# Kernel tuning notes

Measured on AMD Instinct MI355X. Metric: run time of the kernel, lower is better.

## Reference

```python
import jax, jax.numpy as jnp
import numpy as np

EPS = 1e-5

def _ln(x, g, b):
    mu = jnp.mean(x, -1, keepdims=True)
    var = jnp.mean((x - mu) ** 2, -1, keepdims=True)
    return (x - mu) / jnp.sqrt(var + EPS) * g + b

def _edge_scores(x, lat, mask, sn_g, sn_b, tn_g, tn_b, su_w, su_b, tp_w, tp_b, m1_w, m1_b, m2_w, m2_b):
    # x: [B,S,D], lat: [B,K,D] -> edges [B,S,K]
    s = _ln(x, sn_g, sn_b) @ su_w + su_b      # [B,S,E]
    t = _ln(lat, tn_g, tn_b) @ tp_w + tp_b    # [B,K,E]
    B, S, E = s.shape
    K = t.shape[1]
    s4 = jnp.broadcast_to(s[:, :, None, :], (B, S, K, E))
    t4 = jnp.broadcast_to(t[:, None, :, :], (B, S, K, E))
    pair = jnp.concatenate([s4, t4, s4 * t4], axis=-1)  # [B,S,K,3E]
    h = jax.nn.gelu(pair @ m1_w + m1_b, approximate=False)
    e = (h @ m2_w + m2_b)[..., 0]             # [B,S,K]
    e = e / (1.0 + jnp.abs(e))                # softsign
    return e * mask[:, :, None]

def setup_inputs() -> dict:
    key = jax.random.key(0)
    B, St, Si, K, D, E = 2, 2048, 1024, 64, 768, 256
    ks = iter(jax.random.split(key, 64))
    d = {}
    d['text_values'] = jax.random.normal(next(ks), (B, St, D), jnp.float32)
    d['image_values'] = jax.random.normal(next(ks), (B, Si, D), jnp.float32)
    d['latent_state_init'] = jax.random.normal(next(ks), (B, K, D), jnp.float32)
    d['latent_value_init'] = jax.random.normal(next(ks), (B, K, D), jnp.float32)
    d['text_mask'] = jnp.ones((B, St), jnp.float32)
    d['image_mask'] = jnp.ones((B, Si), jnp.float32)
    def scorer(prefix):
        d[prefix + 'sn_g'] = jnp.ones((D,), jnp.float32)
        d[prefix + 'sn_b'] = jnp.zeros((D,), jnp.float32)
        d[prefix + 'tn_g'] = jnp.ones((D,), jnp.float32)
        d[prefix + 'tn_b'] = jnp.zeros((D,), jnp.float32)
        d[prefix + 'su_w'] = jax.random.normal(next(ks), (D, E), jnp.float32) * 0.02
        d[prefix + 'su_b'] = jnp.zeros((E,), jnp.float32)
        d[prefix + 'tp_w'] = jax.random.normal(next(ks), (D, E), jnp.float32) * 0.02
        d[prefix + 'tp_b'] = jnp.zeros((E,), jnp.float32)
        d[prefix + 'm1_w'] = jax.random.normal(next(ks), (3 * E, E), jnp.float32) * 0.02
        d[prefix + 'm1_b'] = jnp.zeros((E,), jnp.float32)
        d[prefix + 'm2_w'] = jax.random.normal(next(ks), (E, 1), jnp.float32) * 0.02
        d[prefix + 'm2_b'] = jnp.zeros((1,), jnp.float32)
    scorer('t_')
    scorer('i_')
    for p in ['tsn', 'isn', 'stn', 'vn']:
        d[p + '_g'] = jnp.ones((D,), jnp.float32)
        d[p + '_b'] = jnp.zeros((D,), jnp.float32)
    d['tsp_w'] = jax.random.normal(next(ks), (D, D), jnp.float32) * 0.02
    d['tsp_b'] = jnp.zeros((D,), jnp.float32)
    d['isp_w'] = jax.random.normal(next(ks), (D, D), jnp.float32) * 0.02
    d['isp_b'] = jnp.zeros((D,), jnp.float32)
    return d

def reference(text_values, image_values, latent_state_init, latent_value_init, text_mask, image_mask,
              t_sn_g, t_sn_b, t_tn_g, t_tn_b, t_su_w, t_su_b, t_tp_w, t_tp_b, t_m1_w, t_m1_b, t_m2_w, t_m2_b,
              i_sn_g, i_sn_b, i_tn_g, i_tn_b, i_su_w, i_su_b, i_tp_w, i_tp_b, i_m1_w, i_m1_b, i_m2_w, i_m2_b,
              tsn_g, tsn_b, isn_g, isn_b, stn_g, stn_b, vn_g, vn_b, tsp_w, tsp_b, isp_w, isp_b):
    t2l = _edge_scores(text_values, latent_value_init, text_mask,
                       t_sn_g, t_sn_b, t_tn_g, t_tn_b, t_su_w, t_su_b, t_tp_w, t_tp_b, t_m1_w, t_m1_b, t_m2_w, t_m2_b)
    i2l = _edge_scores(image_values, latent_value_init, image_mask,
                       i_sn_g, i_sn_b, i_tn_g, i_tn_b, i_su_w, i_su_b, i_tp_w, i_tp_b, i_m1_w, i_m1_b, i_m2_w, i_m2_b)
    tsf = _ln(text_values, tsn_g, tsn_b) @ tsp_w + tsp_b    # [B,St,D]
    isf = _ln(image_values, isn_g, isn_b) @ isp_w + isp_b   # [B,Si,D]
    state_raw = jnp.einsum('bsk,bsd->bkd', t2l, tsf) + jnp.einsum('bsk,bsd->bkd', i2l, isf)
    value_raw = jnp.einsum('bsk,bsd->bkd', t2l, text_values) + jnp.einsum('bsk,bsd->bkd', i2l, image_values)
    latent_state = _ln(state_raw + latent_state_init, stn_g, stn_b)
    latent_value = _ln(value_raw + latent_value_init, vn_g, vn_b)
    return latent_state, latent_value, t2l, i2l
```

## Files before the change

### kernel.cpp

```cpp
#include <hip/hip_runtime.h>
#include <math.h>

#define EPS_LN 1e-5f

#define B_  2
#define ST_ 2048
#define SI_ 1024
#define K_  64
#define D_  768
#define E_  256

typedef __bf16 bf16x8 __attribute__((ext_vector_type(8)));
typedef float  f32x4  __attribute__((ext_vector_type(4)));
typedef unsigned short ushort_t;

__device__ inline ushort_t f2bf(float x) {
    unsigned int u = __float_as_uint(x);
    unsigned int r = (u + 0x7FFFu + ((u >> 16) & 1u)) >> 16;
    return (ushort_t)r;
}

__device__ inline float gelu_fast(float z) {
    float a = fabsf(z);
    float t = __expf(a * -1.702f);
    float r = __builtin_amdgcn_rcpf(1.0f + t);
    float th = fmaf(t * r, -2.0f, 1.0f);
    return fmaf(0.5f * a, th, 0.5f * z);
}

__device__ void sgemm_acc_body(char* smem, int tid,
    const float* A, const float* Bm, const float* rowScale,
    const float* muA, const float* sdA, int so,
    float acc[4][4], int bx, int by, int k0beg, int k0end, int Kd, int N)
{
    float (*As)[65] = (float(*)[65])smem;
    float (*Bs)[64] = (float(*)[64])(smem + 16 * 65 * 4);
    int tx = tid & 15, ty = tid >> 4;
    int row0 = by * 64;
    int col0 = bx * 64;
    for (int k0 = k0beg; k0 < k0end; k0 += 16) {
        {
            int e = tid * 4;
            int r = e >> 4, kk = e & 15;
            float4 av = *(const float4*)(A + (size_t)(row0 + r) * Kd + k0 + kk);
            if (muA) {
                float m = muA[so + row0 + r], sd = sdA[so + row0 + r];
                av.x = (av.x - m) * sd; av.y = (av.y - m) * sd;
                av.z = (av.z - m) * sd; av.w = (av.w - m) * sd;
            }
            As[kk + 0][r] = av.x; As[kk + 1][r] = av.y; As[kk + 2][r] = av.z; As[kk + 3][r] = av.w;
        }
        {
            int e = tid * 4;
            int kk = e >> 6, c = e & 63;
            float4 bv = *(const float4*)(Bm + (size_t)(k0 + kk) * N + col0 + c);
            if (rowScale) {
                float sc = rowScale[k0 + kk];
                bv.x *= sc; bv.y *= sc; bv.z *= sc; bv.w *= sc;
            }
            *(float4*)&Bs[kk][c] = bv;
        }
        __syncthreads();
        #pragma unroll
        for (int kk = 0; kk < 16; ++kk) {
            float a[4], b[4];
            #pragma unroll
            for (int i = 0; i < 4; ++i) a[i] = As[kk][ty + 16 * i];
            #pragma unroll
            for (int j = 0; j < 4; ++j) b[j] = Bs[kk][tx + 16 * j];
            #pragma unroll
            for (int i = 0; i < 4; ++i)
                #pragma unroll
                for (int j = 0; j < 4; ++j)
                    acc[i][j] += a[i] * b[j];
        }
        __syncthreads();
    }
}

__global__ __launch_bounds__(256) void prelude_kernel(
    const float* __restrict__ xt, const float* __restrict__ xi,
    const float* __restrict__ lat,
    float* __restrict__ mu, float* __restrict__ rstd,
    const float* b0, const float* W0, const float* w0, float* f0,
    const float* b1, const float* W1, const float* w1, float* f1,
    const float* b2, const float* W2, const float* w2, float* f2,
    const float* b3, const float* W3, const float* w3, float* f3,
    const float* b4, const float* W4, const float* w4, float* f4,
    const float* b5, const float* W5, const float* w5, float* f5,
    const float* __restrict__ Wsu_t, const float* __restrict__ g_t, ushort_t* __restrict__ WF_t,
    const float* __restrict__ Wsu_i, const float* __restrict__ g_i, ushort_t* __restrict__ WF_i,
    const float* __restrict__ t_tp_w, const float* __restrict__ t_tn_g,
    const float* __restrict__ b_tp_t, float* __restrict__ t_t,
    const float* __restrict__ i_tp_w, const float* __restrict__ i_tn_g,
    const float* __restrict__ b_tp_i, float* __restrict__ t_i,
    float* __restrict__ rs_t, float* __restrict__ rs_i)
{
    extern __shared__ __align__(16) char smem[];
    int bid = blockIdx.x;
    int tid = threadIdx.x;
    if (bid < 16) {
        int bx = bid & 3, by = (bid >> 2) & 1, cfg = bid >> 3;
        float* smu = (float*)(smem + 8256);
        float* srs = smu + 64;
        int row0 = by * 64;
        {
            int r = tid >> 2, part = tid & 3;
            const float* xr = lat + (size_t)(row0 + r) * D_ + part * 192;
            float s = 0.f, q = 0.f;
            for (int i = 0; i < 192; i += 4) {
                float4 v = *(const float4*)(xr + i);
                s += v.x + v.y + v.z + v.w;
                q += v.x * v.x + v.y * v.y + v.z * v.z + v.w * v.w;
            }
            s += __shfl_xor(s, 1, 64); q += __shfl_xor(q, 1, 64);
            s += __shfl_xor(s, 2, 64); q += __shfl_xor(q, 2, 64);
            if (part == 0) {
                float m = s / (float)D_;
                smu[r] = m;
                srs[r] = rsqrtf(q / (float)D_ - m * m + EPS_LN);
            }
        }
        __syncthreads();
        float acc[4][4] = {};
        sgemm_acc_body(smem, tid, lat, cfg ? i_tp_w : t_tp_w, cfg ? i_tn_g : t_tn_g,
                       smu, srs, -row0, acc, bx, by, 0, D_, D_, E_);
        const float* bias = cfg ? b_tp_i : b_tp_t;
        float* C = cfg ? t_i : t_t;
        int tx = tid & 15, ty = tid >> 4;
        #pragma unroll
        for (int i = 0; i < 4; ++i) {
            int r = row0 + ty + 16 * i;
            #pragma unroll
            for (int j = 0; j < 4; ++j) {
                int c = bx * 64 + tx + 16 * j;
                C[(size_t)r * E_ + c] = acc[i][j] + bias[c];
            }
        }
        return;
    }
    if (bid < 56) {
        int f = bid - 16;
        int cfg, ebx;
        if (f < 16) { cfg = f >> 2; ebx = f & 3; }
        else { f -= 16; cfg = 4 + f / 12; ebx = f % 12; }
        const float* blns[6] = {b0, b1, b2, b3, b4, b5};
        const float* Ws[6]   = {W0, W1, W2, W3, W4, W5};
        const float* wbs[6]  = {w0, w1, w2, w3, w4, w5};
        float* bfs[6]        = {f0, f1, f2, f3, f4, f5};
        int E = (cfg >= 4) ? 768 : 256;
        const float* bln = blns[cfg];
        const float* W = Ws[cfg];
        float (*red)[64] = (float(*)[64])smem;
        int c = tid & 63, part = tid >> 6;
        int e = ebx * 64 + c;
        float s = 0.f;
        for (int d = part * 192; d < part * 192 + 192; ++d)
            s += bln[d] * W[(size_t)d * E + e];
        red[part][c] = s; __syncthreads();
        if (part == 0) {
            float v = red[0][c] + red[1][c] + red[2][c] + red[3][c];
            if (wbs[cfg]) v += wbs[cfg][e];
            bfs[cfg][e] = v;
        }
        return;
    }
    if (bid < 248) {
        const int HALF = (D_ >> 5) * (E_ >> 4) * 64;
        int gidx = (bid - 56) * 256 + tid;
        int isImg = gidx >= HALF;
        int idx = isImg ? gidx - HALF : gidx;
        const float* W = isImg ? Wsu_i : Wsu_t;
        const float* g = isImg ? g_i : g_t;
        ushort_t* out = isImg ? WF_i : WF_t;
        int lane = idx & 63;
        int ntile = (idx >> 6) & 15;
        int c = idx >> 10;
        int n = ntile * 16 + (lane & 15);
        int k0 = c * 32 + (lane >> 4) * 8;
        ushort_t o[8];
        #pragma unroll
        for (int j = 0; j < 8; ++j) {
            int k = k0 + j;
            o[j] = f2bf(W[(size_t)k * E_ + n] * g[k]);
        }
        *reinterpret_cast<uint4*>(out + (size_t)idx * 8) = *reinterpret_cast<uint4*>(o);
        return;
    }
    if (bid < 1784) {
        int rb = bid - 248;
        int w = tid >> 6, lane = tid & 63;
        int row = rb * 4 + w;
        const float* src = (row < 4096) ? xt + (size_t)row * D_
                                        : xi + (size_t)(row - 4096) * D_;
        float s = 0.f, q = 0.f;
        #pragma unroll
        for (int rep = 0; rep < 3; ++rep) {
            float4 v = *(const float4*)(src + lane * 4 + rep * 256);
            s += v.x + v.y + v.z + v.w;
            q += v.x * v.x + v.y * v.y + v.z * v.z + v.w * v.w;
        }
        #pragma unroll
        for (int off = 32; off > 0; off >>= 1) {
            s += __shfl_xor(s, off, 64);
            q += __shfl_xor(q, off, 64);
        }
        if (lane == 0) {
            float m = s / (float)D_;
            mu[row] = m;
            rstd[row] = rsqrtf(q / (float)D_ - m * m + EPS_LN);
        }
        return;
    }
    if (tid < 128) rs_t[tid] = 0.f;
    else rs_i[tid - 128] = 0.f;
}

__global__ __launch_bounds__(256) void bigpack_kernel(
    const float* __restrict__ t_t, const float* __restrict__ t_i,
    const float* __restrict__ t_m1_w, const float* __restrict__ t_m1_b,
    const float* __restrict__ i_m1_w, const float* __restrict__ i_m1_b,
    float* __restrict__ c2_t, float* __restrict__ c2_i,
    const float* __restrict__ xt, const float* __restrict__ xi,
    const float* __restrict__ mu, const float* __restrict__ rstd,
    const ushort_t* __restrict__ WF_t, const float* __restrict__ b_su_t, ushort_t* __restrict__ sF_t,
    const ushort_t* __restrict__ WF_i, const float* __restrict__ b_su_i, ushort_t* __restrict__ sF_i,
    ushort_t* __restrict__ XrF_t, ushort_t* __restrict__ XhF_t,
    ushort_t* __restrict__ XrF_i, ushort_t* __restrict__ XhF_i,
    ushort_t* __restrict__ MF_t, ushort_t* __restrict__ MF_i)
{
    extern __shared__ __align__(16) char smem[];
    int bid = blockIdx.x;
    int tid = threadIdx.x;
    if (bid < 16) {
        int bx = bid & 3, by = (bid >> 2) & 1, cfg = bid >> 3;
        float acc[4][4] = {};
        sgemm_acc_body(smem, tid, cfg ? t_i : t_t,
                       (cfg ? i_m1_w : t_m1_w) + (size_t)E_ * E_, nullptr,
                       nullptr, nullptr, 0, acc, bx, by, 0, E_, E_, E_);
        const float* bias = cfg ? i_m1_b : t_m1_b;
        float* C = cfg ? c2_i : c2_t;
        int tx = tid & 15, ty = tid >> 4;
        #pragma unroll
        for (int i = 0; i < 4; ++i) {
            int r = by * 64 + ty + 16 * i;
            #pragma unroll
            for (int j = 0; j < 4; ++j) {
                int c = bx * 64 + tx + 16 * j;
                C[(size_t)r * E_ + c] = acc[i][j] + bias[c];
            }
        }
        return;
    }
    if (bid < 208) {
        int bx = bid - 16;
        int isImg = bx >= 128;
        const float* xsrc = isImg ? xi : xt;
        const ushort_t* BF = isImg ? WF_i : WF_t;
        const float* bias = isImg ? b_su_i : b_su_t;
        ushort_t* sF = isImg ? sF_i : sF_t;
        const float* muP = mu + (isImg ? 4096 : 0);
        const float* rsP = rstd + (isImg ? 4096 : 0);
        int tile0 = (isImg ? bx - 128 : bx) * 2;
        ushort_t* lsbase = (ushort_t*)smem;
        int w = tid >> 6, lane = tid & 63;
        int quad = lane >> 4, n16 = lane & 15;
        int row[2]; float rmu[2], rrs[2];
        #pragma unroll
        for (int mt = 0; mt < 2; ++mt) {
            row[mt] = (tile0 + mt) * 16 + n16;
            rmu[mt] = muP[row[mt]];
            rrs[mt] = rsP[row[mt]];
        }
        f32x4 acc[2][4];
        #pragma unroll
        for (int mt = 0; mt < 2; ++mt)
            #pragma unroll
            for (int nt = 0; nt < 4; ++nt)
                acc[mt][nt] = (f32x4){0.f, 0.f, 0.f, 0.f};
        for (int c = 0; c < 24; ++c) {
            bf16x8 af[2], bf[4];
            #pragma unroll
            for (int mt = 0; mt < 2; ++mt) {
                const float* p = xsrc + (size_t)row[mt] * D_ + c * 32 + quad * 8;
                float4 a = *(const float4*)p;
                float4 b = *(const float4*)(p + 4);
                ushort_t o8[8] = {
                    f2bf((a.x - rmu[mt]) * rrs[mt]), f2bf((a.y - rmu[mt]) * rrs[mt]),
                    f2bf((a.z - rmu[mt]) * rrs[mt]), f2bf((a.w - rmu[mt]) * rrs[mt]),
                    f2bf((b.x - rmu[mt]) * rrs[mt]), f2bf((b.y - rmu[mt]) * rrs[mt]),
                    f2bf((b.z - rmu[mt]) * rrs[mt]), f2bf((b.w - rmu[mt]) * rrs[mt]) };
                af[mt] = *reinterpret_cast<bf16x8*>(o8);
            }
            #pragma unroll
            for (int nt = 0; nt < 4; ++nt)
                bf[nt] = *reinterpret_cast<const bf16x8*>(BF + ((size_t)c * 16 + w * 4 + nt) * 512 + lane * 8);
            #pragma unroll
            for (int mt = 0; mt < 2; ++mt)
                #pragma unroll
                for (int nt = 0; nt < 4; ++nt)
                    acc[mt][nt] = __builtin_amdgcn_mfma_f32_16x16x32_bf16(af[mt], bf[nt], acc[mt][nt], 0, 0, 0);
        }
        #pragma unroll
        for (int mt = 0; mt < 2; ++mt)
            #pragma unroll
            for (int nt = 0; nt < 4; ++nt) {
                float bv = bias[w * 64 + nt * 16 + n16];
                #pragma unroll
                for (int r = 0; r < 4; ++r)
                    lsbase[(w * 32 + mt * 16 + quad * 4 + r) * 72 + nt * 16 + n16] = f2bf(acc[mt][nt][r] + bv);
            }
        __syncthreads();
        #pragma unroll
        for (int mt = 0; mt < 2; ++mt)
            #pragma unroll
            for (int h = 0; h < 2; ++h) {
                uint4 v = *reinterpret_cast<const uint4*>(&lsbase[(w * 32 + mt * 16 + n16) * 72 + h * 32 + quad * 8]);
                *reinterpret_cast<uint4*>(sF + ((size_t)(tile0 + mt) * 8 + 2 * w + h) * 512 + lane * 8) = v;
            }
        return;
    }
    if (bid < 1360) {
        int f = bid - 208;
        int bx = f % 96, by = f / 96;
        float (*tile)[65] = (float(*)[65])smem;
        float* mu_s = (float*)(smem + 64 * 65 * 4);
        float* rs_s = mu_s + 64;
        int isImg = bx >= 64;
        const float* x = isImg ? xi : xt;
        ushort_t* XrF = isImg ? XrF_i : XrF_t;
        ushort_t* XhF = isImg ? XhF_i : XhF_t;
        int rbase = (isImg ? bx - 64 : bx) * 64;
        int statOff = isImg ? 4096 : 0;
        int d0 = by * 64;
        int t = tid;
        #pragma unroll
        for (int rep = 0; rep < 4; ++rep) {
            int rl = (t >> 4) + rep * 16;
            int c4 = (t & 15) * 4;
            *(float4*)&tile[rl][c4] = *(const float4*)(x + (size_t)(rbase + rl) * D_ + d0 + c4);
        }
        if (t < 64) { mu_s[t] = mu[statOff + rbase + t]; rs_s[t] = rstd[statOff + rbase + t]; }
        __syncthreads();
        int lane = t & 63;
        #pragma unroll
        for (int rep = 0; rep < 2; ++rep) {
            int idx = t + rep * 256;
            int nt = (idx >> 6) & 3, cl = (idx >> 8) & 1;
            int kl = cl * 32 + (lane >> 4) * 8;
            int nl = nt * 16 + (lane & 15);
            ushort_t orw[8], oh[8];
            #pragma unroll
            for (int j = 0; j < 8; ++j) {
                float v = tile[kl + j][nl];
                orw[j] = f2bf(v);
                oh[j]  = f2bf((v - mu_s[kl + j]) * rs_s[kl + j]);
            }
            size_t chunk = (size_t)((rbase >> 5) + cl);
            size_t o = ((chunk * 48 + (d0 >> 4) + nt) * 64 + lane) * 8;
            *reinterpret_cast<uint4*>(XrF + o) = *reinterpret_cast<uint4*>(orw);
            *reinterpret_cast<uint4*>(XhF + o) = *reinterpret_cast<uint4*>(oh);
        }
        return;
    }
    {
        const int HALF = B_ * K_ * 16 * 8 * 64;
        int gidx = (bid - 1360) * 256 + tid;
        int isImg = gidx >= HALF;
        int idx = isImg ? gidx - HALF : gidx;
        const float* tP = isImg ? t_i : t_t;
        const float* W3 = (isImg ? i_m1_w : t_m1_w) + 2 * (size_t)E_ * E_;
        const float* W1 = isImg ? i_m1_w : t_m1_w;
        ushort_t* MF = isImg ? MF_i : MF_t;
        int lane = idx & 63;
        int kc = (idx >> 6) & 7;
        int nt = (idx >> 9) & 15;
        int bk = idx >> 13;
        int n = nt * 16 + (lane & 15);
        int e0 = kc * 32 + (lane >> 4) * 8;
        ushort_t out[8];
        #pragma unroll
        for (int j = 0; j < 8; ++j) {
            int e = e0 + j;
            float v = tP[(size_t)bk * E_ + e] * W3[(size_t)e * E_ + n] + W1[(size_t)e * E_ + n];
            out[j] = f2bf(v);
        }
        *reinterpret_cast<uint4*>(MF + (size_t)idx * 8) = *reinterpret_cast<uint4*>(out);
    }
}

__global__ __launch_bounds__(256, 4) void cross_mfma_kernel(
    const ushort_t* __restrict__ sF_t, const ushort_t* __restrict__ MF_t,
    const float* __restrict__ c2_t, const float* __restrict__ m2w_t,
    const float* __restrict__ m2b_t, const float* __restrict__ mask_t,
    float* __restrict__ Et,
    const ushort_t* __restrict__ sF_i, const ushort_t* __restrict__ MF_i,
    const float* __restrict__ c2_i, const float* __restrict__ m2w_i,
    const float* __restrict__ m2b_i, const float* __restrict__ mask_i,
    float* __restrict__ Ei)
{
    int k = blockIdx.x;
    int by = blockIdx.y;
    int isImg = by >= 32;
    int S = isImg ? SI_ : ST_;
    const ushort_t* sF = isImg ? sF_i : sF_t;
    const ushort_t* MF = isImg ? MF_i : MF_t;
    const float* c2P = isImg ? c2_i : c2_t;
    const float* m2w = isImg ? m2w_i : m2w_t;
    const float* m2b = isImg ? m2b_i : m2b_t;
    const float* mask = isImg ? mask_i : mask_t;
    float* Etmp = isImg ? Ei : Et;
    int s0 = (isImg ? by - 32 : by) * 64;
    int b = blockIdx.z;
    int tid = threadIdx.x;
    int w = tid >> 6, lane = tid & 63;
    int quad = lane >> 4, n16 = lane & 15;

    const ushort_t* aBase = sF + (size_t)(b * (S / 16) + (s0 >> 4)) * 4096;
    const ushort_t* bBase = MF + ((size_t)(b * K_ + k) * 16 + w * 4) * 4096;

    f32x4 acc[4][4];
    #pragma unroll
    for (int mt = 0; mt < 4; ++mt)
        #pragma unroll
        for (int nt = 0; nt < 4; ++nt)
            acc[mt][nt] = (f32x4){0.f, 0.f, 0.f, 0.f};

    #pragma unroll
    for (int kc = 0; kc < 8; ++kc) {
        bf16x8 bfr[4], af[4];
        #pragma unroll
        for (int nt = 0; nt < 4; ++nt)
            bfr[nt] = *reinterpret_cast<const bf16x8*>(bBase + (size_t)nt * 4096 + kc * 512 + lane * 8);
        #pragma unroll
        for (int mt = 0; mt < 4; ++mt)
            af[mt] = *reinterpret_cast<const bf16x8*>(aBase + (size_t)mt * 4096 + kc * 512 + lane * 8);
        #pragma unroll
        for (int mt = 0; mt < 4; ++mt)
            #pragma unroll
            for (int nt = 0; nt < 4; ++nt)
                acc[mt][nt] = __builtin_amdgcn_mfma_f32_16x16x32_bf16(af[mt], bfr[nt], acc[mt][nt], 0, 0, 0);
    }

    const float* c2v = c2P + (size_t)(b * K_ + k) * E_;
    float c2r[4], m2r[4];
    #pragma unroll
    for (int nt = 0; nt < 4; ++nt) {
        int col = w * 64 + nt * 16 + n16;
        c2r[nt] = c2v[col];
        m2r[nt] = m2w[col];
    }
    __shared__ float pPart[4][64];
    #pragma unroll
    for (int mt = 0; mt < 4; ++mt) {
        #pragma unroll
        for (int r = 0; r < 4; ++r) {
            float p = 0.f;
            #pragma unroll
            for (int nt = 0; nt < 4; ++nt) {
                float z = acc[mt][nt][r] + c2r[nt];
                p += gelu_fast(z) * m2r[nt];
            }
            p += __shfl_xor(p, 1, 64);
            p += __shfl_xor(p, 2, 64);
            p += __shfl_xor(p, 4, 64);
            p += __shfl_xor(p, 8, 64);
            if (n16 == 0) pPart[w][mt * 16 + quad * 4 + r] = p;
        }
    }
    __syncthreads();
    if (tid < 64) {
        float e = pPart[0][tid] + pPart[1][tid] + pPart[2][tid] + pPart[3][tid] + m2b[0];
        e = e / (1.0f + fabsf(e));
        int srow = s0 + tid;
        e *= mask[(size_t)b * S + srow];
        Etmp[(size_t)(b * K_ + k) * S + srow] = e;
    }
}

__global__ __launch_bounds__(256, 4) void einsum_mfma_kernel(
    const float* __restrict__ Et, const ushort_t* __restrict__ XhF_t,
    const ushort_t* __restrict__ XrF_t, float* __restrict__ PtG, float* __restrict__ PtR,
    const float* __restrict__ Ei, const ushort_t* __restrict__ XhF_i,
    const ushort_t* __restrict__ XrF_i, float* __restrict__ PiG, float* __restrict__ PiR,
    float* __restrict__ t2l, float* __restrict__ i2l,
    float* __restrict__ rs_t, float* __restrict__ rs_i)
{
    __shared__ float tile[64][33];
    int bz = blockIdx.z;
    int isImg = bz >= 2;
    int b = isImg ? bz - 2 : bz;
    int S = isImg ? SI_ : ST_;
    const float* Esrc = isImg ? Ei : Et;
    const ushort_t* XhF = isImg ? XhF_i : XhF_t;
    const ushort_t* XrF = isImg ? XrF_i : XrF_t;
    float* PG = isImg ? PiG : PtG;
    float* PR = isImg ? PiR : PtR;
    int chunksPerBlock = isImg ? 2 : 4;

    int w = threadIdx.x >> 6, lane = threadIdx.x & 63;
    int quad = lane >> 4, n16 = lane & 15;
    int y = blockIdx.y;
    int nt0 = blockIdx.x * 8 + w * 2;
    size_t cb = (size_t)(b * S) / 32 + (size_t)y * chunksPerBlock;

    f32x4 aG[4][2], aR[4][2];
    #pragma unroll
    for (int mt = 0; mt < 4; ++mt)
        #pragma unroll
        for (int nt = 0; nt < 2; ++nt) {
            aG[mt][nt] = (f32x4){0.f, 0.f, 0.f, 0.f};
            aR[mt][nt] = (f32x4){0.f, 0.f, 0.f, 0.f};
        }

    for (int cc = 0; cc < chunksPerBlock; ++cc) {
        size_t c = cb + cc;
        int s0 = (y * chunksPerBlock + cc) * 32;
        bf16x8 af[4], bh[2], bx[2];
        #pragma unroll
        for (int mt = 0; mt < 4; ++mt) {
            int kk = mt * 16 + n16;
            const float* p = Esrc + (size_t)(b * K_ + kk) * S + s0 + quad * 8;
            float4 a = *(const float4*)p;
            float4 bb4 = *(const float4*)(p + 4);
            ushort_t o8[8] = { f2bf(a.x), f2bf(a.y), f2bf(a.z), f2bf(a.w),
                               f2bf(bb4.x), f2bf(bb4.y), f2bf(bb4.z), f2bf(bb4.w) };
            af[mt] = *reinterpret_cast<bf16x8*>(o8);
        }
        #pragma unroll
        for (int nt = 0; nt < 2; ++nt) {
            bh[nt] = *reinterpret_cast<const bf16x8*>(XhF + ((c * 48 + nt0 + nt) * 64 + lane) * 8);
            bx[nt] = *reinterpret_cast<const bf16x8*>(XrF + ((c * 48 + nt0 + nt) * 64 + lane) * 8);
        }
        #pragma unroll
        for (int mt = 0; mt < 4; ++mt)
            #pragma unroll
            for (int nt = 0; nt < 2; ++nt) {
                aG[mt][nt] = __builtin_amdgcn_mfma_f32_16x16x32_bf16(af[mt], bh[nt], aG[mt][nt], 0, 0, 0);
                aR[mt][nt] = __builtin_amdgcn_mfma_f32_16x16x32_bf16(af[mt], bx[nt], aR[mt][nt], 0, 0, 0);
            }
    }
    #pragma unroll
    for (int mt = 0; mt < 4; ++mt)
        #pragma unroll
        for (int nt = 0; nt < 2; ++nt) {
            int d = (nt0 + nt) * 16 + n16;
            #pragma unroll
            for (int r = 0; r < 4; ++r) {
                int krow = mt * 16 + quad * 4 + r;
                size_t o = (((size_t)y * B_ + b) * K_ + krow) * D_ + d;
                PG[o] = aG[mt][nt][r];
                PR[o] = aR[mt][nt][r];
            }
        }

    if (blockIdx.x == 0) {
        float* dst = isImg ? i2l : t2l;
        float* rsum = isImg ? rs_i : rs_t;
        int t = threadIdx.x;
        float ksum = 0.f;
        for (int cc = 0; cc < chunksPerBlock; ++cc) {
            int s0 = (y * chunksPerBlock + cc) * 32;
            {
                int kk = t >> 2, si = (t & 3) * 8;
                const float* p = Esrc + (size_t)(b * K_ + kk) * S + s0 + si;
                *(float4*)&tile[kk][si] = *(const float4*)p;
                *(float4*)&tile[kk][si + 4] = *(const float4*)(p + 4);
            }
            __syncthreads();
            {
                int s = t >> 3, k0 = (t & 7) * 8;
                float o[8];
                #pragma unroll
                for (int j = 0; j < 8; ++j) o[j] = tile[k0 + j][s];
                float* p = dst + ((size_t)b * S + s0 + s) * K_ + k0;
                *(float4*)p = *(float4*)&o[0];
                *(float4*)(p + 4) = *(float4*)&o[4];
            }
            if (t < 64) {
                #pragma unroll
                for (int j = 0; j < 32; ++j) ksum += tile[t][j];
            }
            __syncthreads();
        }
        if (t < 64) atomicAdd(&rsum[b * K_ + t], ksum);
    }
}

__global__ __launch_bounds__(256) void reduce_parts_kernel(
    const float* __restrict__ PtG, const float* __restrict__ PtR,
    const float* __restrict__ PiG, const float* __restrict__ PiR,
    float* __restrict__ Gt, float* __restrict__ Gi, float* __restrict__ Racc,
    float* __restrict__ state_tmp)
{
    const int BKD = B_ * K_ * D_;
    int idx = blockIdx.x * 256 + threadIdx.x;
    if (idx >= BKD) return;
    float gt = 0.f, gi = 0.f, r = 0.f;
    #pragma unroll
    for (int c = 0; c < 16; ++c) { gt += PtG[(size_t)c * BKD + idx]; r += PtR[(size_t)c * BKD + idx]; }
    #pragma unroll
    for (int c = 0; c < 16; ++c) { gi += PiG[(size_t)c * BKD + idx]; r += PiR[(size_t)c * BKD + idx]; }
    Gt[idx] = gt; Gi[idx] = gi; Racc[idx] = r;
    state_tmp[idx] = 0.f;
}

__global__ __launch_bounds__(256) void sgemm3_kernel(
    const float* __restrict__ Gt, const float* __restrict__ tsp_w, const float* __restrict__ tsn_g,
    const float* __restrict__ Gi, const float* __restrict__ isp_w, const float* __restrict__ isn_g,
    float* __restrict__ state_tmp)
{
    extern __shared__ __align__(16) char smem[];
    int f = blockIdx.x;
    int bx = f % 12, by = (f / 12) % 2, z = f / 24;
    int cfg = (z >= 6) ? 1 : 0;
    int kz = cfg ? z - 6 : z;
    float acc[4][4] = {};
    sgemm_acc_body(smem, threadIdx.x,
                   cfg ? Gi : Gt, cfg ? isp_w : tsp_w, cfg ? isn_g : tsn_g,
                   nullptr, nullptr, 0, acc, bx, by, kz * 128, kz * 128 + 128, D_, D_);
    int tx = threadIdx.x & 15, ty = threadIdx.x >> 4;
    #pragma unroll
    for (int i = 0; i < 4; ++i) {
        int r = by * 64 + ty + 16 * i;
        #pragma unroll
        for (int j = 0; j < 4; ++j) {
            int c = bx * 64 + tx + 16 * j;
            atomicAdd(&state_tmp[(size_t)r * D_ + c], acc[i][j]);
        }
    }
}

__global__ __launch_bounds__(256) void final_ln_kernel(
    const float* __restrict__ stateTmp, const float* __restrict__ Racc,
    const float* __restrict__ rs_t, const float* __restrict__ rs_i,
    const float* __restrict__ b_tspf, const float* __restrict__ b_ispf,
    const float* __restrict__ state_init, const float* __restrict__ value_init,
    const float* __restrict__ stn_g, const float* __restrict__ stn_b,
    const float* __restrict__ vn_g, const float* __restrict__ vn_b,
    float* __restrict__ outState, float* __restrict__ outValue)
{
    __shared__ float pre[D_];
    __shared__ float red[256];
    int idx = blockIdx.x;
    int row = idx & 127;
    int isVal = idx >> 7;
    int tid = threadIdx.x;
    if (!isVal) {
        float rt = rs_t[row], ri = rs_i[row];
        for (int d = tid; d < D_; d += 256)
            pre[d] = stateTmp[(size_t)row * D_ + d] + rt * b_tspf[d] + ri * b_ispf[d]
                   + state_init[(size_t)row * D_ + d];
    } else {
        for (int d = tid; d < D_; d += 256)
            pre[d] = Racc[(size_t)row * D_ + d] + value_init[(size_t)row * D_ + d];
    }
    __syncthreads();
    float s = 0.f;
    for (int d = tid; d < D_; d += 256) s += pre[d];
    red[tid] = s; __syncthreads();
    for (int off = 128; off > 0; off >>= 1) { if (tid < off) red[tid] += red[tid + off]; __syncthreads(); }
    float mu = red[0] / (float)D_;
    __syncthreads();
    float v = 0.f;
    for (int d = tid; d < D_; d += 256) { float t = pre[d] - mu; v += t * t; }
    red[tid] = v; __syncthreads();
    for (int off = 128; off > 0; off >>= 1) { if (tid < off) red[tid] += red[tid + off]; __syncthreads(); }
    float rstd = rsqrtf(red[0] / (float)D_ + EPS_LN);
    const float* g  = isVal ? vn_g : stn_g;
    const float* bb = isVal ? vn_b : stn_b;
    float* o = (isVal ? outValue : outState) + (size_t)row * D_;
    for (int d = tid; d < D_; d += 256) o[d] = (pre[d] - mu) * rstd * g[d] + bb[d];
}

extern "C" void kernel_launch(void* const* d_in, const int* in_sizes, int n_in,
                              void* d_out, int out_size, void* d_ws, size_t ws_size,
                              hipStream_t stream) {
    const float* text_values  = (const float*)d_in[0];
    const float* image_values = (const float*)d_in[1];
    const float* lstate_init  = (const float*)d_in[2];
    const float* lvalue_init  = (const float*)d_in[3];
    const float* text_mask    = (const float*)d_in[4];
    const float* image_mask   = (const float*)d_in[5];
    const float* t_sn_g = (const float*)d_in[6];
    const float* t_sn_b = (const float*)d_in[7];
    const float* t_tn_g = (const float*)d_in[8];
    const float* t_tn_b = (const float*)d_in[9];
    const float* t_su_w = (const float*)d_in[10];
    const float* t_su_b = (const float*)d_in[11];
    const float* t_tp_w = (const float*)d_in[12];
    const float* t_tp_b = (const float*)d_in[13];
    const float* t_m1_w = (const float*)d_in[14];
    const float* t_m1_b = (const float*)d_in[15];
    const float* t_m2_w = (const float*)d_in[16];
    const float* t_m2_b = (const float*)d_in[17];
    const float* i_sn_g = (const float*)d_in[18];
    const float* i_sn_b = (const float*)d_in[19];
    const float* i_tn_g = (const float*)d_in[20];
    const float* i_tn_b = (const float*)d_in[21];
    const float* i_su_w = (const float*)d_in[22];
    const float* i_su_b = (const float*)d_in[23];
    const float* i_tp_w = (const float*)d_in[24];
    const float* i_tp_b = (const float*)d_in[25];
    const float* i_m1_w = (const float*)d_in[26];
    const float* i_m1_b = (const float*)d_in[27];
    const float* i_m2_w = (const float*)d_in[28];
    const float* i_m2_b = (const float*)d_in[29];
    const float* tsn_g = (const float*)d_in[30];
    const float* tsn_b = (const float*)d_in[31];
    const float* isn_g = (const float*)d_in[32];
    const float* isn_b = (const float*)d_in[33];
    const float* stn_g = (const float*)d_in[34];
    const float* stn_b = (const float*)d_in[35];
    const float* vn_g  = (const float*)d_in[36];
    const float* vn_b  = (const float*)d_in[37];
    const float* tsp_w = (const float*)d_in[38];
    const float* tsp_b = (const float*)d_in[39];
    const float* isp_w = (const float*)d_in[40];
    const float* isp_b = (const float*)d_in[41];

    float* ws = (float*)d_ws;
    size_t o = 0;
    float* stats_mu = ws + o; o += 6272;
    float* stats_rs = ws + o; o += 6272;
    float* b_su_t = ws + o; o += E_;
    float* b_su_i = ws + o; o += E_;
    float* b_tp_t = ws + o; o += E_;
    float* b_tp_i = ws + o; o += E_;
    float* b_tspf = ws + o; o += D_;
    float* b_ispf = ws + o; o += D_;
    float* t_t  = ws + o; o += (size_t)B_ * K_ * E_;
    float* t_i  = ws + o; o += (size_t)B_ * K_ * E_;
    float* c2_t = ws + o; o += (size_t)B_ * K_ * E_;
    float* c2_i = ws + o; o += (size_t)B_ * K_ * E_;
    float* state_tmp = ws + o; o += (size_t)B_ * K_ * D_;
    float* rs_t = ws + o; o += 128;
    float* rs_i = ws + o; o += 128;
    float* Etmp_t = ws + o; o += (size_t)B_ * K_ * ST_;
    float* Etmp_i = ws + o; o += (size_t)B_ * K_ * SI_;
    ushort_t* WsuF_t = (ushort_t*)(ws + o); o += (size_t)D_ * E_ / 2;
    ushort_t* WsuF_i = (ushort_t*)(ws + o); o += (size_t)D_ * E_ / 2;
    ushort_t* sF_t = (ushort_t*)(ws + o); o += (size_t)B_ * ST_ * E_ / 2;
    ushort_t* sF_i = (ushort_t*)(ws + o); o += (size_t)B_ * SI_ * E_ / 2;
    ushort_t* MF_t = (ushort_t*)(ws + o); o += (size_t)B_ * K_ * E_ * E_ / 2;
    ushort_t* MF_i = (ushort_t*)(ws + o); o += (size_t)B_ * K_ * E_ * E_ / 2;
    ushort_t* XhF_t = (ushort_t*)(ws + o); o += (size_t)B_ * ST_ * D_ / 2;
    ushort_t* XhF_i = (ushort_t*)(ws + o); o += (size_t)B_ * SI_ * D_ / 2;
    ushort_t* XrF_t = (ushort_t*)(ws + o); o += (size_t)B_ * ST_ * D_ / 2;
    ushort_t* XrF_i = (ushort_t*)(ws + o); o += (size_t)B_ * SI_ * D_ / 2;
    const int BKD = B_ * K_ * D_;
    float* PtG = ws + o; o += (size_t)16 * BKD;
    float* PtR = ws + o; o += (size_t)16 * BKD;
    float* PiG = ws + o; o += (size_t)16 * BKD;
    float* PiR = ws + o; o += (size_t)16 * BKD;
    float* Gt   = ws + o; o += BKD;
    float* Gi   = ws + o; o += BKD;
    float* Racc = ws + o; o += BKD;

    float* outState = (float*)d_out;
    float* outValue = (float*)d_out + (size_t)B_ * K_ * D_;
    float* t2l = (float*)d_out + 2 * (size_t)B_ * K_ * D_;
    float* i2l = t2l + (size_t)B_ * ST_ * K_;

    prelude_kernel<<<1785, 256, 8768, stream>>>(
        text_values, image_values, lvalue_init, stats_mu, stats_rs,
        t_sn_b, t_su_w, t_su_b, b_su_t,
        i_sn_b, i_su_w, i_su_b, b_su_i,
        t_tn_b, t_tp_w, t_tp_b, b_tp_t,
        i_tn_b, i_tp_w, i_tp_b, b_tp_i,
        tsn_b, tsp_w, tsp_b, b_tspf,
        isn_b, isp_w, isp_b, b_ispf,
        t_su_w, t_sn_g, WsuF_t,
        i_su_w, i_sn_g, WsuF_i,
        t_tp_w, t_tn_g, b_tp_t, t_t,
        i_tp_w, i_tn_g, b_tp_i, t_i,
        rs_t, rs_i);

    bigpack_kernel<<<9552, 256, 18432, stream>>>(
        t_t, t_i, t_m1_w, t_m1_b, i_m1_w, i_m1_b, c2_t, c2_i,
        text_values, image_values, stats_mu, stats_rs,
        WsuF_t, b_su_t, sF_t,
        WsuF_i, b_su_i, sF_i,
        XrF_t, XhF_t, XrF_i, XhF_i,
        MF_t, MF_i);

    cross_mfma_kernel<<<dim3(K_, 48, B_), 256, 0, stream>>>(
        sF_t, MF_t, c2_t, t_m2_w, t_m2_b, text_mask, Etmp_t,
        sF_i, MF_i, c2_i, i_m2_w, i_m2_b, image_mask, Etmp_i);

    einsum_mfma_kernel<<<dim3(6, 16, 4), 256, 0, stream>>>(
        Etmp_t, XhF_t, XrF_t, PtG, PtR,
        Etmp_i, XhF_i, XrF_i, PiG, PiR,
        t2l, i2l, rs_t, rs_i);

    reduce_parts_kernel<<<(BKD + 255) / 256, 256, 0, stream>>>(
        PtG, PtR, PiG, PiR, Gt, Gi, Racc, state_tmp);

    sgemm3_kernel<<<288, 256, 8256, stream>>>(
        Gt, tsp_w, tsn_g, Gi, isp_w, isn_g, state_tmp);

    final_ln_kernel<<<2 * B_ * K_, 256, 0, stream>>>(
        state_tmp, Racc, rs_t, rs_i, b_tspf, b_ispf,
        lstate_init, lvalue_init, stn_g, stn_b, vn_g, vn_b, outState, outValue);
}
```

Measured before the change: 391.5 us.

## Prepack normalized activations and edge scores into MFMA fragment layout

Splits the old pack kernel into a transpose/pack kernel that also writes the normalized input in bf16 MFMA fragment order (AF), and a stage3 kernel whose su GEMM loads those fragments directly instead of normalizing and converting fp32 rows in its inner loop. It also adds a packE2 kernel that transposes edge scores into the outputs, packs them as bf16 fragments and accumulates row sums, so the einsum kernel no longer converts fp32 edge scores or serializes the transpose in its x==0 blocks. The cost is two extra launches and an extra bf16 copy of the activations written to and read back from memory.

New measurement: 383.3 us. 1.02x faster.

```diff
diff --git a/kernel.cpp b/kernel.cpp
--- a/kernel.cpp
+++ b/kernel.cpp
@@ -216,17 +216,79 @@
     else rs_i[tid - 128] = 0.f;
 }
 
-__global__ __launch_bounds__(256) void bigpack_kernel(
+__global__ __launch_bounds__(256) void tpack_kernel(
+    const float* __restrict__ xt, const float* __restrict__ xi,
+    const float* __restrict__ mu, const float* __restrict__ rstd,
+    ushort_t* __restrict__ XrF_t, ushort_t* __restrict__ XhF_t, ushort_t* __restrict__ AF_t,
+    ushort_t* __restrict__ XrF_i, ushort_t* __restrict__ XhF_i, ushort_t* __restrict__ AF_i)
+{
+    extern __shared__ __align__(16) char smem[];
+    float (*tile)[65] = (float(*)[65])smem;
+    float* mu_s = (float*)(smem + 64 * 65 * 4);
+    float* rs_s = mu_s + 64;
+    int bid = blockIdx.x;
+    int bx = bid % 96, by = bid / 96;
+    int isImg = bx >= 64;
+    const float* x = isImg ? xi : xt;
+    ushort_t* XrF = isImg ? XrF_i : XrF_t;
+    ushort_t* XhF = isImg ? XhF_i : XhF_t;
+    ushort_t* AF  = isImg ? AF_i  : AF_t;
+    int rbase = (isImg ? bx - 64 : bx) * 64;
+    int statOff = isImg ? 4096 : 0;
+    int d0 = by * 64;
+    int t = threadIdx.x;
+    #pragma unroll
+    for (int rep = 0; rep < 4; ++rep) {
+        int rl = (t >> 4) + rep * 16;
+        int c4 = (t & 15) * 4;
+        *(float4*)&tile[rl][c4] = *(const float4*)(x + (size_t)(rbase + rl) * D_ + d0 + c4);
+    }
+    if (t < 64) { mu_s[t] = mu[statOff + rbase + t]; rs_s[t] = rstd[statOff + rbase + t]; }
+    __syncthreads();
+    int lane = t & 63;
+    #pragma unroll
+    for (int rep = 0; rep < 2; ++rep) {
+        int idx = t + rep * 256;
+        int nt = (idx >> 6) & 3, cl = (idx >> 8) & 1;
+        int kl = cl * 32 + (lane >> 4) * 8;
+        int nl = nt * 16 + (lane & 15);
+        ushort_t orw[8], oh[8];
+        #pragma unroll
+        for (int j = 0; j < 8; ++j) {
+            float v = tile[kl + j][nl];
+            orw[j] = f2bf(v);
+            oh[j]  = f2bf((v - mu_s[kl + j]) * rs_s[kl + j]);
+        }
+        size_t chunk = (size_t)((rbase >> 5) + cl);
+        size_t o = ((chunk * 48 + (d0 >> 4) + nt) * 64 + lane) * 8;
+        *reinterpret_cast<uint4*>(XrF + o) = *reinterpret_cast<uint4*>(orw);
+        *reinterpret_cast<uint4*>(XhF + o) = *reinterpret_cast<uint4*>(oh);
+    }
+    #pragma unroll
+    for (int rep = 0; rep < 2; ++rep) {
+        int idx = t + rep * 256;
+        int cl = (idx >> 6) & 1, tl = idx >> 7;
+        int rl = tl * 16 + (lane & 15);
+        int dl = cl * 32 + (lane >> 4) * 8;
+        float m = mu_s[rl], rs = rs_s[rl];
+        ushort_t o8[8];
+        #pragma unroll
+        for (int j = 0; j < 8; ++j)
+            o8[j] = f2bf((tile[rl][dl + j] - m) * rs);
+        size_t o = (((size_t)(rbase >> 4) + tl) * 24 + (d0 >> 5) + cl) * 512 + lane * 8;
+        *reinterpret_cast<uint4*>(AF + o) = *reinterpret_cast<uint4*>(o8);
+    }
+}
+
+__global__ __launch_bounds__(256) void stage3_kernel(
     const float* __restrict__ t_t, const float* __restrict__ t_i,
     const float* __restrict__ t_m1_w, const float* __restrict__ t_m1_b,
     const float* __restrict__ i_m1_w, const float* __restrict__ i_m1_b,
     float* __restrict__ c2_t, float* __restrict__ c2_i,
-    const float* __restrict__ xt, const float* __restrict__ xi,
-    const float* __restrict__ mu, const float* __restrict__ rstd,
-    const ushort_t* __restrict__ WF_t, const float* __restrict__ b_su_t, ushort_t* __restrict__ sF_t,
-    const ushort_t* __restrict__ WF_i, const float* __restrict__ b_su_i, ushort_t* __restrict__ sF_i,
-    ushort_t* __restrict__ XrF_t, ushort_t* __restrict__ XhF_t,
-    ushort_t* __restrict__ XrF_i, ushort_t* __restrict__ XhF_i,
+    const ushort_t* __restrict__ AF_t, const ushort_t* __restrict__ BF_t,
+    const float* __restrict__ b_su_t, ushort_t* __restrict__ sF_t,
+    const ushort_t* __restrict__ AF_i, const ushort_t* __restrict__ BF_i,
+    const float* __restrict__ b_su_i, ushort_t* __restrict__ sF_i,
     ushort_t* __restrict__ MF_t, ushort_t* __restrict__ MF_i)
 {
     extern __shared__ __align__(16) char smem[];
@@ -255,23 +317,14 @@
     if (bid < 208) {
         int bx = bid - 16;
         int isImg = bx >= 128;
-        const float* xsrc = isImg ? xi : xt;
-        const ushort_t* BF = isImg ? WF_i : WF_t;
+        const ushort_t* AF = isImg ? AF_i : AF_t;
+        const ushort_t* BF = isImg ? BF_i : BF_t;
         const float* bias = isImg ? b_su_i : b_su_t;
         ushort_t* sF = isImg ? sF_i : sF_t;
-        const float* muP = mu + (isImg ? 4096 : 0);
-        const float* rsP = rstd + (isImg ? 4096 : 0);
         int tile0 = (isImg ? bx - 128 : bx) * 2;
         ushort_t* lsbase = (ushort_t*)smem;
         int w = tid >> 6, lane = tid & 63;
         int quad = lane >> 4, n16 = lane & 15;
-        int row[2]; float rmu[2], rrs[2];
-        #pragma unroll
-        for (int mt = 0; mt < 2; ++mt) {
-            row[mt] = (tile0 + mt) * 16 + n16;
-            rmu[mt] = muP[row[mt]];
-            rrs[mt] = rsP[row[mt]];
-        }
         f32x4 acc[2][4];
         #pragma unroll
         for (int mt = 0; mt < 2; ++mt)
@@ -281,17 +334,8 @@
         for (int c = 0; c < 24; ++c) {
             bf16x8 af[2], bf[4];
             #pragma unroll
-            for (int mt = 0; mt < 2; ++mt) {
-                const float* p = xsrc + (size_t)row[mt] * D_ + c * 32 + quad * 8;
-                float4 a = *(const float4*)p;
-                float4 b = *(const float4*)(p + 4);
-                ushort_t o8[8] = {
-                    f2bf((a.x - rmu[mt]) * rrs[mt]), f2bf((a.y - rmu[mt]) * rrs[mt]),
-                    f2bf((a.z - rmu[mt]) * rrs[mt]), f2bf((a.w - rmu[mt]) * rrs[mt]),
-                    f2bf((b.x - rmu[mt]) * rrs[mt]), f2bf((b.y - rmu[mt]) * rrs[mt]),
-                    f2bf((b.z - rmu[mt]) * rrs[mt]), f2bf((b.w - rmu[mt]) * rrs[mt]) };
-                af[mt] = *reinterpret_cast<bf16x8*>(o8);
-            }
+            for (int mt = 0; mt < 2; ++mt)
+                af[mt] = *reinterpret_cast<const bf16x8*>(AF + ((size_t)(tile0 + mt) * 24 + c) * 512 + lane * 8);
             #pragma unroll
             for (int nt = 0; nt < 4; ++nt)
                 bf[nt] = *reinterpret_cast<const bf16x8*>(BF + ((size_t)c * 16 + w * 4 + nt) * 512 + lane * 8);
@@ -320,52 +364,9 @@
             }
         return;
     }
-    if (bid < 1360) {
-        int f = bid - 208;
-        int bx = f % 96, by = f / 96;
-        float (*tile)[65] = (float(*)[65])smem;
-        float* mu_s = (float*)(smem + 64 * 65 * 4);
-        float* rs_s = mu_s + 64;
-        int isImg = bx >= 64;
-        const float* x = isImg ? xi : xt;
-        ushort_t* XrF = isImg ? XrF_i : XrF_t;
-        ushort_t* XhF = isImg ? XhF_i : XhF_t;
-        int rbase = (isImg ? bx - 64 : bx) * 64;
-        int statOff = isImg ? 4096 : 0;
-        int d0 = by * 64;
-        int t = tid;
-        #pragma unroll
-        for (int rep = 0; rep < 4; ++rep) {
-            int rl = (t >> 4) + rep * 16;
-            int c4 = (t & 15) * 4;
-            *(float4*)&tile[rl][c4] = *(const float4*)(x + (size_t)(rbase + rl) * D_ + d0 + c4);
-        }
-        if (t < 64) { mu_s[t] = mu[statOff + rbase + t]; rs_s[t] = rstd[statOff + rbase + t]; }
-        __syncthreads();
-        int lane = t & 63;
-        #pragma unroll
-        for (int rep = 0; rep < 2; ++rep) {
-            int idx = t + rep * 256;
-            int nt = (idx >> 6) & 3, cl = (idx >> 8) & 1;
-            int kl = cl * 32 + (lane >> 4) * 8;
-            int nl = nt * 16 + (lane & 15);
-            ushort_t orw[8], oh[8];
-            #pragma unroll
-            for (int j = 0; j < 8; ++j) {
-                float v = tile[kl + j][nl];
-                orw[j] = f2bf(v);
-                oh[j]  = f2bf((v - mu_s[kl + j]) * rs_s[kl + j]);
-            }
-            size_t chunk = (size_t)((rbase >> 5) + cl);
-            size_t o = ((chunk * 48 + (d0 >> 4) + nt) * 64 + lane) * 8;
-            *reinterpret_cast<uint4*>(XrF + o) = *reinterpret_cast<uint4*>(orw);
-            *reinterpret_cast<uint4*>(XhF + o) = *reinterpret_cast<uint4*>(oh);
-        }
-        return;
-    }
     {
         const int HALF = B_ * K_ * 16 * 8 * 64;
-        int gidx = (bid - 1360) * 256 + tid;
+        int gidx = (bid - 208) * 256 + tid;
         int isImg = gidx >= HALF;
         int idx = isImg ? gidx - HALF : gidx;
         const float* tP = isImg ? t_i : t_t;
@@ -478,20 +479,69 @@
     }
 }
 
+__global__ __launch_bounds__(256) void packE2_kernel(
+    const float* __restrict__ Et, const float* __restrict__ Ei,
+    float* __restrict__ t2l, float* __restrict__ i2l,
+    ushort_t* __restrict__ EF_t, ushort_t* __restrict__ EF_i,
+    float* __restrict__ rs_t, float* __restrict__ rs_i)
+{
+    __shared__ float tile[64][33];
+    int g = blockIdx.x;
+    int isImg = g >= 128;
+    const float* Esrc = isImg ? Ei : Et;
+    float* dst = isImg ? i2l : t2l;
+    ushort_t* EF = isImg ? EF_i : EF_t;
+    float* rsum = isImg ? rs_i : rs_t;
+    int chunk = isImg ? g - 128 : g;
+    int S = isImg ? SI_ : ST_;
+    int b = (chunk * 32) / S;
+    int s0 = (chunk * 32) % S;
+    int t = threadIdx.x;
+    {
+        int k = t >> 2, si = (t & 3) * 8;
+        const float* p = Esrc + (size_t)(b * K_ + k) * S + s0 + si;
+        *(float4*)&tile[k][si] = *(const float4*)p;
+        *(float4*)&tile[k][si + 4] = *(const float4*)(p + 4);
+    }
+    __syncthreads();
+    {
+        int s = t >> 3, k0 = (t & 7) * 8;
+        float o[8];
+        #pragma unroll
+        for (int j = 0; j < 8; ++j) o[j] = tile[k0 + j][s];
+        float* p = dst + ((size_t)b * S + s0 + s) * K_ + k0;
+        *(float4*)p = *(float4*)&o[0];
+        *(float4*)(p + 4) = *(float4*)&o[4];
+    }
+    {
+        int mt = t >> 6, lane = t & 63;
+        int k = mt * 16 + (lane & 15);
+        int sl0 = (lane >> 4) * 8;
+        ushort_t o8[8];
+        #pragma unroll
+        for (int j = 0; j < 8; ++j)
+            o8[j] = f2bf(tile[k][sl0 + j]);
+        *reinterpret_cast<uint4*>(EF + (((size_t)chunk * 4 + mt) * 64 + lane) * 8) = *reinterpret_cast<uint4*>(o8);
+    }
+    if (t < 64) {
+        float s = 0.f;
+        #pragma unroll
+        for (int j = 0; j < 32; ++j) s += tile[t][j];
+        atomicAdd(&rsum[b * K_ + t], s);
+    }
+}
+
 __global__ __launch_bounds__(256, 4) void einsum_mfma_kernel(
-    const float* __restrict__ Et, const ushort_t* __restrict__ XhF_t,
+    const ushort_t* __restrict__ EF_t, const ushort_t* __restrict__ XhF_t,
     const ushort_t* __restrict__ XrF_t, float* __restrict__ PtG, float* __restrict__ PtR,
-    const float* __restrict__ Ei, const ushort_t* __restrict__ XhF_i,
-    const ushort_t* __restrict__ XrF_i, float* __restrict__ PiG, float* __restrict__ PiR,
-    float* __restrict__ t2l, float* __restrict__ i2l,
-    float* __restrict__ rs_t, float* __restrict__ rs_i)
-{
-    __shared__ float tile[64][33];
+    const ushort_t* __restrict__ EF_i, const ushort_t* __restrict__ XhF_i,
+    const ushort_t* __restrict__ XrF_i, float* __restrict__ PiG, float* __restrict__ PiR)
+{
     int bz = blockIdx.z;
     int isImg = bz >= 2;
     int b = isImg ? bz - 2 : bz;
     int S = isImg ? SI_ : ST_;
-    const float* Esrc = isImg ? Ei : Et;
+    const ushort_t* EF = isImg ? EF_i : EF_t;
     const ushort_t* XhF = isImg ? XhF_i : XhF_t;
     const ushort_t* XrF = isImg ? XrF_i : XrF_t;
     float* PG = isImg ? PiG : PtG;
@@ -515,18 +565,10 @@
 
     for (int cc = 0; cc < chunksPerBlock; ++cc) {
         size_t c = cb + cc;
-        int s0 = (y * chunksPerBlock + cc) * 32;
         bf16x8 af[4], bh[2], bx[2];
         #pragma unroll
-        for (int mt = 0; mt < 4; ++mt) {
-            int kk = mt * 16 + n16;
-            const float* p = Esrc + (size_t)(b * K_ + kk) * S + s0 + quad * 8;
-            float4 a = *(const float4*)p;
-            float4 bb4 = *(const float4*)(p + 4);
-            ushort_t o8[8] = { f2bf(a.x), f2bf(a.y), f2bf(a.z), f2bf(a.w),
-                               f2bf(bb4.x), f2bf(bb4.y), f2bf(bb4.z), f2bf(bb4.w) };
-            af[mt] = *reinterpret_cast<bf16x8*>(o8);
-        }
+        for (int mt = 0; mt < 4; ++mt)
+            af[mt] = *reinterpret_cast<const bf16x8*>(EF + ((c * 4 + mt) * 64 + lane) * 8);
         #pragma unroll
         for (int nt = 0; nt < 2; ++nt) {
             bh[nt] = *reinterpret_cast<const bf16x8*>(XhF + ((c * 48 + nt0 + nt) * 64 + lane) * 8);
@@ -553,38 +595,6 @@
                 PR[o] = aR[mt][nt][r];
             }
         }
-
-    if (blockIdx.x == 0) {
-        float* dst = isImg ? i2l : t2l;
-        float* rsum = isImg ? rs_i : rs_t;
-        int t = threadIdx.x;
-        float ksum = 0.f;
-        for (int cc = 0; cc < chunksPerBlock; ++cc) {
-            int s0 = (y * chunksPerBlock + cc) * 32;
-            {
-                int kk = t >> 2, si = (t & 3) * 8;
-                const float* p = Esrc + (size_t)(b * K_ + kk) * S + s0 + si;
-                *(float4*)&tile[kk][si] = *(const float4*)p;
-                *(float4*)&tile[kk][si + 4] = *(const float4*)(p + 4);
-            }
-            __syncthreads();
-            {
-                int s = t >> 3, k0 = (t & 7) * 8;
-                float o[8];
-                #pragma unroll
-                for (int j = 0; j < 8; ++j) o[j] = tile[k0 + j][s];
-                float* p = dst + ((size_t)b * S + s0 + s) * K_ + k0;
-                *(float4*)p = *(float4*)&o[0];
-                *(float4*)(p + 4) = *(float4*)&o[4];
-            }
-            if (t < 64) {
-                #pragma unroll
-                for (int j = 0; j < 32; ++j) ksum += tile[t][j];
-            }
-            __syncthreads();
-        }
-        if (t < 64) atomicAdd(&rsum[b * K_ + t], ksum);
-    }
 }
 
 __global__ __launch_bounds__(256) void reduce_parts_kernel(
@@ -738,6 +748,8 @@
     float* rs_i = ws + o; o += 128;
     float* Etmp_t = ws + o; o += (size_t)B_ * K_ * ST_;
     float* Etmp_i = ws + o; o += (size_t)B_ * K_ * SI_;
+    ushort_t* AF_t = (ushort_t*)(ws + o); o += (size_t)B_ * ST_ * D_ / 2;
+    ushort_t* AF_i = (ushort_t*)(ws + o); o += (size_t)B_ * SI_ * D_ / 2;
     ushort_t* WsuF_t = (ushort_t*)(ws + o); o += (size_t)D_ * E_ / 2;
     ushort_t* WsuF_i = (ushort_t*)(ws + o); o += (size_t)D_ * E_ / 2;
     ushort_t* sF_t = (ushort_t*)(ws + o); o += (size_t)B_ * ST_ * E_ / 2;
@@ -748,6 +760,8 @@
     ushort_t* XhF_i = (ushort_t*)(ws + o); o += (size_t)B_ * SI_ * D_ / 2;
     ushort_t* XrF_t = (ushort_t*)(ws + o); o += (size_t)B_ * ST_ * D_ / 2;
     ushort_t* XrF_i = (ushort_t*)(ws + o); o += (size_t)B_ * SI_ * D_ / 2;
+    ushort_t* EF_t  = (ushort_t*)(ws + o); o += (size_t)B_ * ST_ * K_ / 2;
+    ushort_t* EF_i  = (ushort_t*)(ws + o); o += (size_t)B_ * SI_ * K_ / 2;
     const int BKD = B_ * K_ * D_;
     float* PtG = ws + o; o += (size_t)16 * BKD;
     float* PtR = ws + o; o += (size_t)16 * BKD;
@@ -776,22 +790,26 @@
         i_tp_w, i_tn_g, b_tp_i, t_i,
         rs_t, rs_i);
 
-    bigpack_kernel<<<9552, 256, 18432, stream>>>(
+    tpack_kernel<<<1152, 256, 17152, stream>>>(
+        text_values, image_values, stats_mu, stats_rs,
+        XrF_t, XhF_t, AF_t, XrF_i, XhF_i, AF_i);
+
+    stage3_kernel<<<8400, 256, 18432, stream>>>(
         t_t, t_i, t_m1_w, t_m1_b, i_m1_w, i_m1_b, c2_t, c2_i,
-        text_values, image_values, stats_mu, stats_rs,
-        WsuF_t, b_su_t, sF_t,
-        WsuF_i, b_su_i, sF_i,
-        XrF_t, XhF_t, XrF_i, XhF_i,
+        AF_t, WsuF_t, b_su_t, sF_t,
+        AF_i, WsuF_i, b_su_i, sF_i,
         MF_t, MF_i);
 
     cross_mfma_kernel<<<dim3(K_, 48, B_), 256, 0, stream>>>(
         sF_t, MF_t, c2_t, t_m2_w, t_m2_b, text_mask, Etmp_t,
         sF_i, MF_i, c2_i, i_m2_w, i_m2_b, image_mask, Etmp_i);
 
+    packE2_kernel<<<192, 256, 0, stream>>>(
+        Etmp_t, Etmp_i, t2l, i2l, EF_t, EF_i, rs_t, rs_i);
+
     einsum_mfma_kernel<<<dim3(6, 16, 4), 256, 0, stream>>>(
-        Etmp_t, XhF_t, XrF_t, PtG, PtR,
-        Etmp_i, XhF_i, XrF_i, PiG, PiR,
-        t2l, i2l, rs_t, rs_i);
+        EF_t, XhF_t, XrF_t, PtG, PtR,
+        EF_i, XhF_i, XrF_i, PiG, PiR);
 
     reduce_parts_kernel<<<(BKD + 255) / 256, 256, 0, stream>>>(
         PtG, PtR, PiG, PiR, Gt, Gi, Racc, state_tmp);
```
